# Performance work log

Measured on AMD Instinct MI355X. Metric: run time of the kernel, lower is better.

## Reference

```python
import jax, jax.numpy as jnp
import numpy as np

N_NODES = 100000
N_EDGES = 1600000
N_GRAPHS = 1024
D = 128
L = 3
BN_EPS = 1e-5


def setup_inputs() -> dict:
    key = jax.random.key(0)
    ks = jax.random.split(key, 16)
    x = jax.random.normal(ks[0], (N_NODES, D), dtype=jnp.float32)
    edge_index = jax.random.randint(ks[1], (2, N_EDGES), 0, N_NODES, dtype=jnp.int64)
    batch = jnp.sort(jax.random.randint(ks[2], (N_NODES,), 0, N_GRAPHS, dtype=jnp.int64))
    w = lambda k, shape: jax.random.normal(k, shape, dtype=jnp.float32) * 0.05
    return {
        "x": x,
        "edge_index": edge_index,
        "batch": batch,
        "conv_W1": w(ks[3], (L, D, D)),
        "conv_b1": w(ks[4], (L, D)),
        "bn_gamma": jax.random.uniform(ks[5], (L, D), dtype=jnp.float32) + 0.5,
        "bn_beta": w(ks[6], (L, D)),
        "bn_mean": w(ks[7], (L, D)),
        "bn_var": jax.random.uniform(ks[8], (L, D), dtype=jnp.float32) + 0.5,
        "conv_W2": w(ks[9], (L, D, D)),
        "conv_b2": w(ks[10], (L, D)),
        "head_W1": w(ks[11], (D, D)),
        "head_b1": w(ks[12], (D,)),
        "head_W2": w(ks[13], (D, D)),
        "head_b2": w(ks[14], (D,)),
    }


def reference(x, edge_index, batch, conv_W1, conv_b1, bn_gamma, bn_beta,
              bn_mean, bn_var, conv_W2, conv_b2, head_W1, head_b1,
              head_W2, head_b2):
    n = x.shape[0]
    src, dst = edge_index[0], edge_index[1]
    for l in range(L):
        # GINConv, eps=0: nn(x + sum_{j->i} x_j)
        agg = jax.ops.segment_sum(x[src], dst, num_segments=n)  # [N, D]
        h = x + agg
        # MLP([in, h, h]): Linear -> BatchNorm(eval) -> ReLU -> Linear
        h = h @ conv_W1[l] + conv_b1[l]
        h = (h - bn_mean[l]) * jax.lax.rsqrt(bn_var[l] + BN_EPS) * bn_gamma[l] + bn_beta[l]
        h = jax.nn.relu(h)
        h = h @ conv_W2[l] + conv_b2[l]
        x = jax.nn.relu(h)  # .relu() in the outer forward
    # global_add_pool over graph ids
    g = jax.ops.segment_sum(x, batch, num_segments=N_GRAPHS)  # [B, D]
    # head MLP (norm=None, dropout inactive at eval): Linear -> ReLU -> Linear
    g = jax.nn.relu(g @ head_W1 + head_b1)
    return g @ head_W2 + head_b2
```

## Files before the change

### kernel.cpp

```cpp
#include <hip/hip_runtime.h>

#define N_NODES  100000
#define N_EDGES  1600000
#define N_GRAPHS 1024
#define D        128
#define BN_EPS   1e-5f

#define FNSLICE      98
#define FSLICE_NODES 1024
#define FSLICE_CAP   20480
#define QCAP         96
#define CCHUNK       4000
#define CGRID        400

typedef short bf16x8 __attribute__((ext_vector_type(8)));
typedef float f32x4  __attribute__((ext_vector_type(4)));

__device__ __forceinline__ ushort f2bf(float f) {
    unsigned int b = __float_as_uint(f);
    return (ushort)((b + 0x7fffu + ((b >> 16) & 1u)) >> 16);
}
__device__ __forceinline__ float bflo(unsigned int u) { return __uint_as_float(u << 16); }
__device__ __forceinline__ float bfhi(unsigned int u) { return __uint_as_float(u & 0xffff0000u); }
__device__ __forceinline__ unsigned int packbf(float x, float y) {
    return (unsigned int)f2bf(x) | ((unsigned int)f2bf(y) << 16);
}


__global__ void zero_kernel(int* __restrict__ p, int n) {
    int i = blockIdx.x * blockDim.x + threadIdx.x;
    if (i < n) p[i] = 0;
}

__global__ __launch_bounds__(256) void compact_kernel(const int* __restrict__ src,
                                                      const int* __restrict__ dst,
                                                      unsigned int* __restrict__ squeue,
                                                      int* __restrict__ slice_tail) {
    __shared__ unsigned int qbuf[FNSLICE * QCAP];
    __shared__ int qcnt[FNSLICE];
    __shared__ int qbase[FNSLICE];
    int t = threadIdx.x;
    for (int i = t; i < FNSLICE; i += 256) qcnt[i] = 0;
    __syncthreads();
    int e0 = blockIdx.x * CCHUNK;
    int eend = e0 + CCHUNK; if (eend > N_EDGES) eend = N_EDGES;
    for (int e = e0 + t; e < eend; e += 256) {
        int d = dst[e], s = src[e];
        int sl = d >> 10;
        unsigned int pk = ((unsigned int)(d & 1023) << 17) | (unsigned int)s;
        int pos = atomicAdd(&qcnt[sl], 1);
        if (pos < QCAP) qbuf[sl * QCAP + pos] = pk;
        else {
            int gp = atomicAdd(&slice_tail[sl], 1);
            squeue[(size_t)sl * FSLICE_CAP + gp] = pk;
        }
    }
    __syncthreads();
    for (int i = t; i < FNSLICE; i += 256) {
        int n = qcnt[i]; if (n > QCAP) n = QCAP;
        qbase[i] = atomicAdd(&slice_tail[i], n);
    }
    __syncthreads();
    for (int sl = 0; sl < FNSLICE; ++sl) {
        int n = qcnt[sl]; if (n > QCAP) n = QCAP;
        int gb = qbase[sl];
        for (int i = t; i < n; i += 256)
            squeue[(size_t)sl * FSLICE_CAP + gb + i] = qbuf[sl * QCAP + i];
    }
}

__global__ __launch_bounds__(128) void slice_scan(const int* __restrict__ slice_tail,
                                                  int* __restrict__ slice_base,
                                                  int* __restrict__ offsets) {
    __shared__ int part[128];
    int t = threadIdx.x;
    int v = (t < FNSLICE) ? slice_tail[t] : 0;
    part[t] = v;
    __syncthreads();
    for (int off = 1; off < 128; off <<= 1) {
        int u = (t >= off) ? part[t - off] : 0;
        __syncthreads();
        part[t] += u;
        __syncthreads();
    }
    if (t < FNSLICE) slice_base[t] = part[t] - v;
    if (t == 0) offsets[N_NODES] = N_EDGES;
}

__global__ __launch_bounds__(1024) void fill_local(const unsigned int* __restrict__ squeue,
                                                   const int* __restrict__ slice_tail,
                                                   const int* __restrict__ slice_base,
                                                   int* __restrict__ offsets,
                                                   int* __restrict__ csr_src) {
    __shared__ int hist[FSLICE_NODES];
    __shared__ int cur[FSLICE_NODES];
    int sl = blockIdx.x, t = threadIdx.x;
    int n = slice_tail[sl];
    size_t qb = (size_t)sl * FSLICE_CAP;
    int gbase = slice_base[sl];
    hist[t] = 0;
    __syncthreads();
    for (int i = t; i < n; i += 1024)
        atomicAdd(&hist[squeue[qb + i] >> 17], 1);
    __syncthreads();
    int v = hist[t];
    for (int off = 1; off < 1024; off <<= 1) {
        int u = (t >= off) ? hist[t - off] : 0;
        __syncthreads();
        hist[t] += u;
        __syncthreads();
    }
    int excl = hist[t] - v;
    cur[t] = excl;
    int node = sl * FSLICE_NODES + t;
    if (node < N_NODES) offsets[node] = gbase + excl;
    __syncthreads();
    for (int i = t; i < n; i += 1024) {
        unsigned int p = squeue[qb + i];
        int slot = atomicAdd(&cur[p >> 17], 1);
        csr_src[gbase + slot] = (int)(p & 0x1FFFFu);
    }
}

__global__ void gstart_kernel(const int* __restrict__ batch, int* __restrict__ gstart) {
    int g = blockIdx.x * blockDim.x + threadIdx.x;
    if (g > N_GRAPHS) return;
    int lo = 0, hi = N_NODES;
    while (lo < hi) {
        int mid = (lo + hi) >> 1;
        if (batch[mid] < g) lo = mid + 1; else hi = mid;
    }
    gstart[g] = lo;
}


__global__ __launch_bounds__(256) void cvt_x_kernel(const float* __restrict__ x,
                                                    ushort* __restrict__ xb) {
    size_t i = ((size_t)blockIdx.x * 256 + threadIdx.x) * 8;
    float4 v0 = *(const float4*)(x + i);
    float4 v1 = *(const float4*)(x + i + 4);
    uint4 o;
    o.x = packbf(v0.x, v0.y); o.y = packbf(v0.z, v0.w);
    o.z = packbf(v1.x, v1.y); o.w = packbf(v1.z, v1.w);
    *(uint4*)(xb + i) = o;
}

__global__ __launch_bounds__(128) void prep_w_kernel(const float* __restrict__ W1,
                                                     const float* __restrict__ W2,
                                                     ushort* __restrict__ Wt) {
    int i = blockIdx.y, k = blockIdx.x, n = threadIdx.x, l = i >> 1;
    const float* W = (i & 1) ? (W2 + (size_t)l * D * D) : (W1 + (size_t)l * D * D);
    Wt[(size_t)i * D * D + n * D + k] = f2bf(W[k * D + n]);
}

__global__ __launch_bounds__(128) void prep_fold_kernel(
        const float* __restrict__ b1, const float* __restrict__ gamma,
        const float* __restrict__ beta, const float* __restrict__ mean,
        const float* __restrict__ var, const float* __restrict__ b2,
        float* __restrict__ folds) {
    int i = blockIdx.x, j = threadIdx.x, l = i >> 1;
    float s, o;
    if ((i & 1) == 0) {
        float sv = gamma[l * D + j] * rsqrtf(var[l * D + j] + BN_EPS);
        s = sv;
        o = (b1[l * D + j] - mean[l * D + j]) * sv + beta[l * D + j];
    } else {
        s = 1.0f;
        o = b2[l * D + j];
    }
    folds[(size_t)i * 2 * D + j]     = s;
    folds[(size_t)i * 2 * D + D + j] = o;
}

__global__ __launch_bounds__(256) void gather_bf16(const ushort* __restrict__ xb,
                                                   const int* __restrict__ offsets,
                                                   const int* __restrict__ csr_src,
                                                   ushort* __restrict__ hb) {
    int wv = threadIdx.x >> 6, lane = threadIdx.x & 63;
    int node = blockIdx.x * 4 + wv;
    const unsigned int* base = (const unsigned int*)xb;
    unsigned int u = base[(size_t)node * 64 + lane];
    float ax = bflo(u), ay = bfhi(u);
    int b = offsets[node], e = offsets[node + 1];
    int i = b;
    for (; i + 7 < e; i += 8) {
        int s0 = csr_src[i],     s1 = csr_src[i + 1], s2 = csr_src[i + 2], s3 = csr_src[i + 3];
        int s4 = csr_src[i + 4], s5 = csr_src[i + 5], s6 = csr_src[i + 6], s7 = csr_src[i + 7];
        unsigned int v0 = base[(size_t)s0 * 64 + lane];
        unsigned int v1 = base[(size_t)s1 * 64 + lane];
        unsigned int v2 = base[(size_t)s2 * 64 + lane];
        unsigned int v3 = base[(size_t)s3 * 64 + lane];
        unsigned int v4 = base[(size_t)s4 * 64 + lane];
        unsigned int v5 = base[(size_t)s5 * 64 + lane];
        unsigned int v6 = base[(size_t)s6 * 64 + lane];
        unsigned int v7 = base[(size_t)s7 * 64 + lane];
        ax += bflo(v0) + bflo(v1) + bflo(v2) + bflo(v3)
            + bflo(v4) + bflo(v5) + bflo(v6) + bflo(v7);
        ay += bfhi(v0) + bfhi(v1) + bfhi(v2) + bfhi(v3)
            + bfhi(v4) + bfhi(v5) + bfhi(v6) + bfhi(v7);
    }
    for (; i + 3 < e; i += 4) {
        int s0 = csr_src[i], s1 = csr_src[i + 1], s2 = csr_src[i + 2], s3 = csr_src[i + 3];
        unsigned int v0 = base[(size_t)s0 * 64 + lane];
        unsigned int v1 = base[(size_t)s1 * 64 + lane];
        unsigned int v2 = base[(size_t)s2 * 64 + lane];
        unsigned int v3 = base[(size_t)s3 * 64 + lane];
        ax += bflo(v0) + bflo(v1) + bflo(v2) + bflo(v3);
        ay += bfhi(v0) + bfhi(v1) + bfhi(v2) + bfhi(v3);
    }
    for (; i < e; ++i) {
        unsigned int v = base[(size_t)csr_src[i] * 64 + lane];
        ax += bflo(v); ay += bfhi(v);
    }
    ((unsigned int*)hb)[(size_t)node * 64 + lane] = packbf(ax, ay);
}

__global__ __launch_bounds__(512) void fused_gemm(const ushort* __restrict__ in,
                                                  ushort* __restrict__ out,
                                                  const ushort* __restrict__ Wt1,
                                                  const ushort* __restrict__ Wt2,
                                                  const float* __restrict__ fold1,
                                                  const float* __restrict__ fold2) {
    __shared__ ushort As[128 * 136];
    __shared__ ushort Bs1[128 * 136];
    __shared__ ushort Bs2[128 * 136];
    ushort* Cs = Bs1;
    int t = threadIdx.x;
    int row0 = blockIdx.x * 128;

#pragma unroll
    for (int i = 0; i < 4; ++i) {
        int f = t + 512 * i; int m = f >> 4, g = f & 15;
        *(float4*)(As + m * 136 + g * 8) = *(const float4*)(in + (size_t)(row0 + m) * D + g * 8);
        *(float4*)(Bs1 + m * 136 + g * 8) = *(const float4*)(Wt1 + (size_t)m * D + g * 8);
        *(float4*)(Bs2 + m * 136 + g * 8) = *(const float4*)(Wt2 + (size_t)m * D + g * 8);
    }
    __syncthreads();

    int lane = t & 63, wv = t >> 6;
    int quad = lane >> 4, mr = lane & 15;
    int mbase = wv * 16;
    const ushort* ap = As + (mbase + mr) * 136 + quad * 8;
    bf16x8 a0 = *(const bf16x8*)(ap);
    bf16x8 a1 = *(const bf16x8*)(ap + 32);
    bf16x8 a2 = *(const bf16x8*)(ap + 64);
    bf16x8 a3 = *(const bf16x8*)(ap + 96);
    __syncthreads();

#pragma unroll
    for (int nt = 0; nt < 8; ++nt) {
        const ushort* bq = Bs1 + (nt * 16 + mr) * 136 + quad * 8;
        bf16x8 b0 = *(const bf16x8*)(bq);
        bf16x8 b1 = *(const bf16x8*)(bq + 32);
        bf16x8 b2 = *(const bf16x8*)(bq + 64);
        bf16x8 b3 = *(const bf16x8*)(bq + 96);
        f32x4 acc = {0.f, 0.f, 0.f, 0.f};
        acc = __builtin_amdgcn_mfma_f32_16x16x32_bf16(a0, b0, acc, 0, 0, 0);
        acc = __builtin_amdgcn_mfma_f32_16x16x32_bf16(a1, b1, acc, 0, 0, 0);
        acc = __builtin_amdgcn_mfma_f32_16x16x32_bf16(a2, b2, acc, 0, 0, 0);
        acc = __builtin_amdgcn_mfma_f32_16x16x32_bf16(a3, b3, acc, 0, 0, 0);
        int j = nt * 16 + mr;
        float s = fold1[j], o = fold1[D + j];
#pragma unroll
        for (int r = 0; r < 4; ++r) {
            float z = fmaxf(fmaf(acc[r], s, o), 0.0f);
            As[(mbase + quad * 4 + r) * 136 + j] = f2bf(z);
        }
    }
    __syncthreads();

    const ushort* hp = As + (mbase + mr) * 136 + quad * 8;
    bf16x8 h0 = *(const bf16x8*)(hp);
    bf16x8 h1 = *(const bf16x8*)(hp + 32);
    bf16x8 h2 = *(const bf16x8*)(hp + 64);
    bf16x8 h3 = *(const bf16x8*)(hp + 96);
#pragma unroll
    for (int nt = 0; nt < 8; ++nt) {
        const ushort* bq = Bs2 + (nt * 16 + mr) * 136 + quad * 8;
        bf16x8 b0 = *(const bf16x8*)(bq);
        bf16x8 b1 = *(const bf16x8*)(bq + 32);
        bf16x8 b2 = *(const bf16x8*)(bq + 64);
        bf16x8 b3 = *(const bf16x8*)(bq + 96);
        f32x4 acc = {0.f, 0.f, 0.f, 0.f};
        acc = __builtin_amdgcn_mfma_f32_16x16x32_bf16(h0, b0, acc, 0, 0, 0);
        acc = __builtin_amdgcn_mfma_f32_16x16x32_bf16(h1, b1, acc, 0, 0, 0);
        acc = __builtin_amdgcn_mfma_f32_16x16x32_bf16(h2, b2, acc, 0, 0, 0);
        acc = __builtin_amdgcn_mfma_f32_16x16x32_bf16(h3, b3, acc, 0, 0, 0);
        int j = nt * 16 + mr;
        float o = fold2[D + j];
#pragma unroll
        for (int r = 0; r < 4; ++r) {
            float z = fmaxf(acc[r] + o, 0.0f);
            Cs[(mbase + quad * 4 + r) * 136 + j] = f2bf(z);
        }
    }
    __syncthreads();

#pragma unroll
    for (int i = 0; i < 8; ++i) {
        int f = t + 512 * i; int lr = f >> 5, g = f & 31;
        if (row0 + lr < N_NODES)
            *(float2*)(out + (size_t)(row0 + lr) * D + g * 4) =
                *(const float2*)(Cs + lr * 136 + g * 4);
    }
}

__global__ __launch_bounds__(128) void pool_kernel(const ushort* __restrict__ xb,
                                                   const int* __restrict__ gstart,
                                                   float* __restrict__ g) {
    int gr = blockIdx.x, j = threadIdx.x;
    float acc = 0.0f;
    int b = gstart[gr], e = gstart[gr + 1];
    for (int i = b; i < e; ++i)
        acc += __uint_as_float(((unsigned int)xb[(size_t)i * D + j]) << 16);
    g[gr * D + j] = acc;
}

__global__ __launch_bounds__(128) void head_kernel(const float* __restrict__ g,
                                                   const float* __restrict__ W1,
                                                   const float* __restrict__ b1,
                                                   const float* __restrict__ W2,
                                                   const float* __restrict__ b2,
                                                   float* __restrict__ out) {
    __shared__ float row[128];
    __shared__ float t1[128];
    int r = blockIdx.x, j = threadIdx.x;
    row[j] = g[r * D + j];
    __syncthreads();
    float acc = b1[j];
    for (int k = 0; k < D; ++k) acc = fmaf(row[k], W1[k * D + j], acc);
    t1[j] = fmaxf(acc, 0.0f);
    __syncthreads();
    float acc2 = b2[j];
    for (int k = 0; k < D; ++k) acc2 = fmaf(t1[k], W2[k * D + j], acc2);
    out[r * D + j] = acc2;
}

extern "C" void kernel_launch(void* const* d_in, const int* in_sizes, int n_in,
                              void* d_out, int out_size, void* d_ws, size_t ws_size,
                              hipStream_t stream) {
    const float* x        = (const float*)d_in[0];
    const int*   ei       = (const int*)d_in[1];
    const int*   src      = ei;
    const int*   dst      = ei + N_EDGES;
    const int*   batch    = (const int*)d_in[2];
    const float* conv_W1  = (const float*)d_in[3];
    const float* conv_b1  = (const float*)d_in[4];
    const float* bn_gamma = (const float*)d_in[5];
    const float* bn_beta  = (const float*)d_in[6];
    const float* bn_mean  = (const float*)d_in[7];
    const float* bn_var   = (const float*)d_in[8];
    const float* conv_W2  = (const float*)d_in[9];
    const float* conv_b2  = (const float*)d_in[10];
    const float* head_W1  = (const float*)d_in[11];
    const float* head_b1  = (const float*)d_in[12];
    const float* head_W2  = (const float*)d_in[13];
    const float* head_b2  = (const float*)d_in[14];
    float* out = (float*)d_out;

    char* ws = (char*)d_ws;
    size_t off = 0;
    auto alloc = [&](size_t bytes) -> void* {
        void* p = ws + off;
        off = (off + bytes + 255) & ~(size_t)255;
        return p;
    };
    const size_t NODE_BUF = (size_t)(N_NODES + 128) * D * sizeof(ushort);
    ushort* buf0    = (ushort*)alloc(NODE_BUF);
    ushort* buf1    = (ushort*)alloc(NODE_BUF);
    ushort* Wt      = (ushort*)alloc((size_t)6 * D * D * sizeof(ushort));
    float*  folds   = (float*)alloc((size_t)6 * 2 * D * sizeof(float));
    unsigned int* squeue = (unsigned int*)alloc((size_t)FNSLICE * FSLICE_CAP * sizeof(unsigned int));
    int*   csr_src  = (int*)alloc((size_t)N_EDGES * sizeof(int));
    int*   offsets  = (int*)alloc((size_t)(N_NODES + 1) * sizeof(int));
    int*   slice_tail = (int*)alloc((size_t)FNSLICE * sizeof(int));
    int*   slice_base = (int*)alloc((size_t)FNSLICE * sizeof(int));
    int*   gstart   = (int*)alloc((size_t)(N_GRAPHS + 1) * sizeof(int));
    float* gpool    = (float*)alloc((size_t)N_GRAPHS * D * sizeof(float));

    zero_kernel<<<1, 128, 0, stream>>>(slice_tail, FNSLICE);
    compact_kernel<<<CGRID, 256, 0, stream>>>(src, dst, squeue, slice_tail);
    slice_scan<<<1, 128, 0, stream>>>(slice_tail, slice_base, offsets);
    fill_local<<<FNSLICE, 1024, 0, stream>>>(squeue, slice_tail, slice_base,
                                             offsets, csr_src);
    gstart_kernel<<<(N_GRAPHS + 1 + 255) / 256, 256, 0, stream>>>(batch, gstart);
    cvt_x_kernel<<<(N_NODES * D) / (256 * 8), 256, 0, stream>>>(x, buf0);
    prep_w_kernel<<<dim3(128, 6), 128, 0, stream>>>(conv_W1, conv_W2, Wt);
    prep_fold_kernel<<<6, 128, 0, stream>>>(conv_b1, bn_gamma, bn_beta,
                                            bn_mean, bn_var, conv_b2, folds);

    const int FUSED_GRID = (N_NODES + 127) / 128;
    for (int l = 0; l < 3; ++l) {
        gather_bf16<<<N_NODES / 4, 256, 0, stream>>>(buf0, offsets, csr_src, buf1);
        fused_gemm<<<FUSED_GRID, 512, 0, stream>>>(buf1, buf0,
            Wt + (size_t)(2 * l) * D * D, Wt + (size_t)(2 * l + 1) * D * D,
            folds + (size_t)(2 * l) * 2 * D, folds + (size_t)(2 * l + 1) * 2 * D);
    }

    pool_kernel<<<N_GRAPHS, 128, 0, stream>>>(buf0, gstart, gpool);
    head_kernel<<<N_GRAPHS, 128, 0, stream>>>(gpool, head_W1, head_b1,
                                              head_W2, head_b2, out);
}
```

Before: 478.6 us.

## Read GEMM weights from global, unroll gather by 16, per-wave queue flush

The fused GEMM no longer stages both weight matrices in shared memory. It reads B fragments straight from global/L2, cutting LDS from three tiles to two and dropping two barriers, which should allow more resident blocks. The gather loop is unrolled to 16 outstanding neighbor loads to raise memory-level parallelism, and the CSR bucket flush now gives each slice to one wavefront instead of looping all slices across the whole block. Removing the barriers relies on each wave touching only its own 16 rows of As. The global weight reads and the extra registers from the wider unroll may offset some of the gains.

```diff
diff --git a/kernel.cpp b/kernel.cpp
--- a/kernel.cpp
+++ b/kernel.cpp
@@ -61,10 +61,11 @@
         qbase[i] = atomicAdd(&slice_tail[i], n);
     }
     __syncthreads();
-    for (int sl = 0; sl < FNSLICE; ++sl) {
+    int wv = t >> 6, ln = t & 63;
+    for (int sl = wv; sl < FNSLICE; sl += 4) {
         int n = qcnt[sl]; if (n > QCAP) n = QCAP;
         int gb = qbase[sl];
-        for (int i = t; i < n; i += 256)
+        for (int i = ln; i < n; i += 64)
             squeue[(size_t)sl * FSLICE_CAP + gb + i] = qbuf[sl * QCAP + i];
     }
 }
@@ -183,9 +184,11 @@
     float ax = bflo(u), ay = bfhi(u);
     int b = offsets[node], e = offsets[node + 1];
     int i = b;
-    for (; i + 7 < e; i += 8) {
-        int s0 = csr_src[i],     s1 = csr_src[i + 1], s2 = csr_src[i + 2], s3 = csr_src[i + 3];
-        int s4 = csr_src[i + 4], s5 = csr_src[i + 5], s6 = csr_src[i + 6], s7 = csr_src[i + 7];
+    for (; i + 15 < e; i += 16) {
+        int s0 = csr_src[i],      s1 = csr_src[i + 1],  s2 = csr_src[i + 2],  s3 = csr_src[i + 3];
+        int s4 = csr_src[i + 4],  s5 = csr_src[i + 5],  s6 = csr_src[i + 6],  s7 = csr_src[i + 7];
+        int s8 = csr_src[i + 8],  s9 = csr_src[i + 9],  sa = csr_src[i + 10], sb = csr_src[i + 11];
+        int sc = csr_src[i + 12], sd = csr_src[i + 13], se = csr_src[i + 14], sf = csr_src[i + 15];
         unsigned int v0 = base[(size_t)s0 * 64 + lane];
         unsigned int v1 = base[(size_t)s1 * 64 + lane];
         unsigned int v2 = base[(size_t)s2 * 64 + lane];
@@ -194,10 +197,22 @@
         unsigned int v5 = base[(size_t)s5 * 64 + lane];
         unsigned int v6 = base[(size_t)s6 * 64 + lane];
         unsigned int v7 = base[(size_t)s7 * 64 + lane];
+        unsigned int v8 = base[(size_t)s8 * 64 + lane];
+        unsigned int v9 = base[(size_t)s9 * 64 + lane];
+        unsigned int va = base[(size_t)sa * 64 + lane];
+        unsigned int vb = base[(size_t)sb * 64 + lane];
+        unsigned int vc = base[(size_t)sc * 64 + lane];
+        unsigned int vd = base[(size_t)sd * 64 + lane];
+        unsigned int ve = base[(size_t)se * 64 + lane];
+        unsigned int vf = base[(size_t)sf * 64 + lane];
         ax += bflo(v0) + bflo(v1) + bflo(v2) + bflo(v3)
-            + bflo(v4) + bflo(v5) + bflo(v6) + bflo(v7);
+            + bflo(v4) + bflo(v5) + bflo(v6) + bflo(v7)
+            + bflo(v8) + bflo(v9) + bflo(va) + bflo(vb)
+            + bflo(vc) + bflo(vd) + bflo(ve) + bflo(vf);
         ay += bfhi(v0) + bfhi(v1) + bfhi(v2) + bfhi(v3)
-            + bfhi(v4) + bfhi(v5) + bfhi(v6) + bfhi(v7);
+            + bfhi(v4) + bfhi(v5) + bfhi(v6) + bfhi(v7)
+            + bfhi(v8) + bfhi(v9) + bfhi(va) + bfhi(vb)
+            + bfhi(vc) + bfhi(vd) + bfhi(ve) + bfhi(vf);
     }
     for (; i + 3 < e; i += 4) {
         int s0 = csr_src[i], s1 = csr_src[i + 1], s2 = csr_src[i + 2], s3 = csr_src[i + 3];
@@ -222,9 +237,7 @@
                                                   const float* __restrict__ fold1,
                                                   const float* __restrict__ fold2) {
     __shared__ ushort As[128 * 136];
-    __shared__ ushort Bs1[128 * 136];
-    __shared__ ushort Bs2[128 * 136];
-    ushort* Cs = Bs1;
+    __shared__ ushort Cs[128 * 136];
     int t = threadIdx.x;
     int row0 = blockIdx.x * 128;
 
@@ -232,8 +245,6 @@
     for (int i = 0; i < 4; ++i) {
         int f = t + 512 * i; int m = f >> 4, g = f & 15;
         *(float4*)(As + m * 136 + g * 8) = *(const float4*)(in + (size_t)(row0 + m) * D + g * 8);
-        *(float4*)(Bs1 + m * 136 + g * 8) = *(const float4*)(Wt1 + (size_t)m * D + g * 8);
-        *(float4*)(Bs2 + m * 136 + g * 8) = *(const float4*)(Wt2 + (size_t)m * D + g * 8);
     }
     __syncthreads();
 
@@ -245,11 +256,10 @@
     bf16x8 a1 = *(const bf16x8*)(ap + 32);
     bf16x8 a2 = *(const bf16x8*)(ap + 64);
     bf16x8 a3 = *(const bf16x8*)(ap + 96);
-    __syncthreads();
 
 #pragma unroll
     for (int nt = 0; nt < 8; ++nt) {
-        const ushort* bq = Bs1 + (nt * 16 + mr) * 136 + quad * 8;
+        const ushort* bq = Wt1 + (size_t)(nt * 16 + mr) * D + quad * 8;
         bf16x8 b0 = *(const bf16x8*)(bq);
         bf16x8 b1 = *(const bf16x8*)(bq + 32);
         bf16x8 b2 = *(const bf16x8*)(bq + 64);
@@ -267,7 +277,6 @@
             As[(mbase + quad * 4 + r) * 136 + j] = f2bf(z);
         }
     }
-    __syncthreads();
 
     const ushort* hp = As + (mbase + mr) * 136 + quad * 8;
     bf16x8 h0 = *(const bf16x8*)(hp);
@@ -276,7 +285,7 @@
     bf16x8 h3 = *(const bf16x8*)(hp + 96);
 #pragma unroll
     for (int nt = 0; nt < 8; ++nt) {
-        const ushort* bq = Bs2 + (nt * 16 + mr) * 136 + quad * 8;
+        const ushort* bq = Wt2 + (size_t)(nt * 16 + mr) * D + quad * 8;
         bf16x8 b0 = *(const bf16x8*)(bq);
         bf16x8 b1 = *(const bf16x8*)(bq + 32);
         bf16x8 b2 = *(const bf16x8*)(bq + 64);
```

Measured after the change: 589.6 us. 23.2% more time.
